# Kernel tuning notes

Hardware: AMD Instinct MI355X
Metric: run time of the kernel (lower is better)

The kernel has to match this reference:

```python
import jax, jax.numpy as jnp
import numpy as np

HEADS = 6
EPS = 1e-5


def _na_idx(L, k, d):
    # NATTEN-style dilated neighborhood: work within dilation cosets,
    # clamp window to stay inside the image (window shifts at borders).
    i = np.arange(L)
    g = i % d
    p = i // d
    Lg = (L - g + d - 1) // d  # coset length per position
    start = np.clip(p - k // 2, 0, Lg - k)
    j = np.arange(k)
    nbr = g[:, None] + d * (start[:, None] + j[None, :])          # [L,k] neighbor coords
    rel = (start[:, None] + j[None, :]) - p[:, None] + (k - 1)    # [L,k] rpb index in [0,2k-2]
    return jnp.asarray(nbr, jnp.int32), jnp.asarray(rel, jnp.int32)


def _na2d(x, qkv_w, qkv_b, proj_w, proj_b, rpb, heads, k, d):
    # x: [B,H,W,C] NHWC neighborhood attention with relative positional bias
    B, H, W, C = x.shape
    dh = C // heads
    scale = dh ** -0.5
    qkv = (x @ qkv_w + qkv_b).reshape(B, H, W, 3, heads, dh)
    qkv = jnp.transpose(qkv, (3, 0, 4, 1, 2, 5))  # [3,B,h,H,W,dh]
    q, kk, v = qkv[0] * scale, qkv[1], qkv[2]
    nh, rh = _na_idx(H, k, d)
    nw, rw = _na_idx(W, k, d)

    def gather(t):  # [B,h,H,W,dh] -> [B,h,H,W,k,k,dh]
        t = t[:, :, nh]              # [B,h,H,k,W,dh]
        t = t[:, :, :, :, nw]        # [B,h,H,k,W,k,dh]
        return jnp.transpose(t, (0, 1, 2, 4, 3, 5, 6))

    kn, vn = gather(kk), gather(v)
    attn = jnp.einsum('bhxyd,bhxyijd->bhxyij', q, kn)  # [B,h,H,W,k,k]
    bias = rpb[:, rh]                  # [h,H,k,2k-1]
    bias = bias[:, :, :, rw]           # [h,H,k,W,k]
    bias = jnp.transpose(bias, (0, 1, 3, 2, 4))  # [h,H,W,k,k]
    attn = attn + bias[None]
    attn = jax.nn.softmax(attn.reshape(B, heads, H, W, k * k), axis=-1)
    attn = attn.reshape(B, heads, H, W, k, k)
    out = jnp.einsum('bhxyij,bhxyijd->bhxyd', attn, vn)
    out = jnp.transpose(out, (0, 2, 3, 1, 4)).reshape(B, H, W, C)
    return out @ proj_w + proj_b


def _rln(x, w, b, m1_w, m1_b, m2_w, m2_b):
    # Revised LayerNorm: normalize over (C,H,W) per sample; meta1/meta2 are 1x1 convs on std/mean
    mean = jnp.mean(x, axis=(1, 2, 3), keepdims=True)
    std = jnp.sqrt(jnp.mean((x - mean) ** 2, axis=(1, 2, 3), keepdims=True) + EPS)
    out = (x - mean) / std * w + b
    rescale = m1_w[None, :, None, None] * std + m1_b[None, :, None, None]
    rebias = m2_w[None, :, None, None] * mean + m2_b[None, :, None, None]
    return out, rescale, rebias


def _c11(x, w, b):  # 1x1 conv on NCHW == per-pixel linear
    return jnp.einsum('bchw,oc->bohw', x, w) + b[None, :, None, None]


def _gelu(x):
    return jax.nn.gelu(x, approximate=False)


def reference(x, ln_w, ln_b, m1_w, m1_b, m2_w, m2_b, qkv1_w, qkv1_b, proj1_w, proj1_b, rpb1, qkv2_w, qkv2_b, proj2_w, proj2_b, rpb2, mlp_w1, mlp_b1, mlp_w2, mlp_b2, bn_g, bn_b, bn_m, bn_v, pa_w1, pa_b1, pa_w2, pa_b2, ca_w1, ca_b1, ca_w2, ca_b2, m2a_w1, m2a_b1, m2a_w2, m2a_b2):
    # ---- NA block 1 (kernel 7, dilation 1) ----
    sc = x
    y, rs, rb = _rln(x, ln_w, ln_b, m1_w, m1_b, m2_w, m2_b)
    a = _na2d(jnp.transpose(y, (0, 2, 3, 1)), qkv1_w, qkv1_b, proj1_w, proj1_b, rpb1, HEADS, 7, 1)
    x = sc + jnp.transpose(a, (0, 3, 1, 2)) * rs + rb
    # ---- NA block 2 (kernel 5, dilation 8) ----
    sc = x
    y, rs, rb = _rln(x, ln_w, ln_b, m1_w, m1_b, m2_w, m2_b)
    a = _na2d(jnp.transpose(y, (0, 2, 3, 1)), qkv2_w, qkv2_b, proj2_w, proj2_b, rpb2, HEADS, 5, 8)
    x = sc + jnp.transpose(a, (0, 3, 1, 2)) * rs + rb
    # ---- MLP (source reuses the pre-attn2 shortcut `sc`) ----
    y, rs, rb = _rln(x, ln_w, ln_b, m1_w, m1_b, m2_w, m2_b)
    m = _c11(jax.nn.relu(_c11(y, mlp_w1, mlp_b1)), mlp_w2, mlp_b2)
    x = sc + m * rs + rb
    # ---- BN + pixel attention + channel attention + mlp2 ----
    sc = x
    inv = jax.lax.rsqrt(bn_v + EPS)
    y = (x - bn_m[None, :, None, None]) * (inv * bn_g)[None, :, None, None] + bn_b[None, :, None, None]
    pa = jax.nn.sigmoid(_c11(_gelu(_c11(y, pa_w1, pa_b1)), pa_w2, pa_b2))  # [B,1,H,W]
    y = pa * y
    gap = jnp.mean(y, axis=(2, 3), keepdims=True)
    ca = jax.nn.sigmoid(_c11(_gelu(_c11(gap, ca_w1, ca_b1)), ca_w2, ca_b2))  # [B,C,1,1]
    y = ca * y
    y = _c11(_gelu(_c11(y, m2a_w1, m2a_b1)), m2a_w2, m2a_b2)
    return sc + y


def setup_inputs() -> dict:
    key = jax.random.key(0)
    B, C, H, W, HID = 4, 96, 64, 64, 384
    ks = iter(jax.random.split(key, 48))

    def rn(shape, s=0.02):
        return jax.random.normal(next(ks), shape, jnp.float32) * s

    d = {}
    d['x'] = jax.random.normal(next(ks), (B, C, H, W), jnp.float32)
    d['ln_w'] = jnp.ones((1, C, 1, 1), jnp.float32)
    d['ln_b'] = jnp.zeros((1, C, 1, 1), jnp.float32)
    d['m1_w'] = rn((C,)); d['m1_b'] = jnp.ones((C,), jnp.float32)
    d['m2_w'] = rn((C,)); d['m2_b'] = jnp.zeros((C,), jnp.float32)
    d['qkv1_w'] = rn((C, 3 * C)); d['qkv1_b'] = jnp.zeros((3 * C,), jnp.float32)
    d['proj1_w'] = rn((C, C)); d['proj1_b'] = jnp.zeros((C,), jnp.float32)
    d['rpb1'] = rn((HEADS, 13, 13))
    d['qkv2_w'] = rn((C, 3 * C)); d['qkv2_b'] = jnp.zeros((3 * C,), jnp.float32)
    d['proj2_w'] = rn((C, C)); d['proj2_b'] = jnp.zeros((C,), jnp.float32)
    d['rpb2'] = rn((HEADS, 9, 9))
    d['mlp_w1'] = rn((HID, C)); d['mlp_b1'] = jnp.zeros((HID,), jnp.float32)
    d['mlp_w2'] = rn((C, HID)); d['mlp_b2'] = jnp.zeros((C,), jnp.float32)
    d['bn_g'] = jnp.ones((C,), jnp.float32); d['bn_b'] = jnp.zeros((C,), jnp.float32)
    d['bn_m'] = jnp.zeros((C,), jnp.float32); d['bn_v'] = jnp.ones((C,), jnp.float32)
    d['pa_w1'] = rn((C // 8, C)); d['pa_b1'] = jnp.zeros((C // 8,), jnp.float32)
    d['pa_w2'] = rn((1, C // 8)); d['pa_b2'] = jnp.zeros((1,), jnp.float32)
    d['ca_w1'] = rn((C, C)); d['ca_b1'] = jnp.zeros((C,), jnp.float32)
    d['ca_w2'] = rn((C, C)); d['ca_b2'] = jnp.zeros((C,), jnp.float32)
    d['m2a_w1'] = rn((C, C)); d['m2a_b1'] = jnp.zeros((C,), jnp.float32)
    d['m2a_w2'] = rn((C, C)); d['m2a_b2'] = jnp.zeros((C,), jnp.float32)
    return d
```

## Files before the change

kernel.cpp:

```cpp
#include <hip/hip_runtime.h>
#include <math.h>

#define CC 96
#define NP 4096
#define NHEADS 6
#define NELEMF 393216.0f
#define EPSF 1e-5f

typedef __attribute__((ext_vector_type(8))) short bf16x8;
typedef __attribute__((ext_vector_type(4))) float f32x4;
#define MFMA16(a,b,c) __builtin_amdgcn_mfma_f32_16x16x32_bf16(a,b,c,0,0,0)

#define WS_STATS 0
#define WQKV1  64
#define WQKV2  (WQKV1+13824)
#define WPROJ1 (WQKV2+13824)
#define WPROJ2 (WPROJ1+4608)
#define WMLP1  (WPROJ2+4608)
#define WMLP2  (WMLP1+18432)
#define WM2A1  (WMLP2+18432)
#define WM2A2  (WM2A1+4608)
#define WPA1T  (WM2A2+4608)
#define WBNS   (WPA1T+1152)
#define WS_YPM 84352
#define WS_Q   870784
#define WS_K   (WS_Q+786432)
#define WS_V   (WS_K+786432)
#define WS_ATTPM (WS_V+786432)
#define WS_X1  (WS_ATTPM+786432)
#define WS_X2  (WS_X1+1572864)
#define WS_X3  (WS_X2+1572864)
#define WS_PA  (WS_X3+1572864)
#define WS_GAP (WS_PA+16384)
#define WS_CA  (WS_GAP+384)

__device__ __forceinline__ float gelu_f(float x){
  return 0.5f * x * (1.0f + erff(x * 0.7071067811865476f));
}
__device__ __forceinline__ float sigmoid_f(float x){
  return 1.0f / (1.0f + __expf(-x));
}
__device__ __forceinline__ unsigned short bfr(float f){
  unsigned int u = __float_as_uint(f);
  u += 0x7fffu + ((u >> 16) & 1u);
  return (unsigned short)(u >> 16);
}
__device__ __forceinline__ unsigned int bfpack(float a, float b){
  return (unsigned int)bfr(a) | ((unsigned int)bfr(b) << 16);
}
__device__ __forceinline__ float bflo(unsigned int u){ return __uint_as_float(u << 16); }
__device__ __forceinline__ float bfhi(unsigned int u){ return __uint_as_float(u & 0xffff0000u); }
__device__ __forceinline__ void get_ms(const float* st, int b, float& mean, float& inv, float& stdv){
  float s = st[b], s2 = st[4+b];
  mean = s * (1.0f/NELEMF);
  float var = fmaxf(s2 * (1.0f/NELEMF) - mean*mean, 0.0f);
  stdv = sqrtf(var + EPSF);
  inv = 1.0f / stdv;
}

__global__ void stats_kernel(const float* __restrict__ src, float* __restrict__ st){
  int b = blockIdx.x / CC, c = blockIdx.x % CC;
  const float* p = src + (b*CC + c)*NP;
  float s = 0.f, s2 = 0.f;
  for(int i = threadIdx.x; i < NP; i += 256){ float v = p[i]; s += v; s2 = fmaf(v, v, s2); }
  for(int off = 32; off > 0; off >>= 1){ s += __shfl_down(s, off); s2 += __shfl_down(s2, off); }
  __shared__ float ls[8];
  int wid = threadIdx.x >> 6;
  if((threadIdx.x & 63) == 0){ ls[wid] = s; ls[4+wid] = s2; }
  __syncthreads();
  if(threadIdx.x == 0){
    atomicAdd(&st[b],   ls[0]+ls[1]+ls[2]+ls[3]);
    atomicAdd(&st[4+b], ls[4]+ls[5]+ls[6]+ls[7]);
  }
}

__global__ void prep_weights(const float* __restrict__ q1, const float* __restrict__ q2,
                             const float* __restrict__ p1, const float* __restrict__ p2,
                             const float* __restrict__ w1, const float* __restrict__ w2,
                             const float* __restrict__ a1, const float* __restrict__ a2,
                             const float* __restrict__ pw1,
                             const float* __restrict__ bg, const float* __restrict__ bb,
                             const float* __restrict__ bm, const float* __restrict__ bv,
                             float* __restrict__ ws){
  int gid = blockIdx.x*256 + threadIdx.x;
  if(gid < 27648){ int n = gid/96, c = gid%96; ((unsigned short*)(ws+WQKV1))[gid] = bfr(q1[c*288+n]); }
  else if(gid < 55296){ int g = gid-27648; int n = g/96, c = g%96; ((unsigned short*)(ws+WQKV2))[g] = bfr(q2[c*288+n]); }
  else if(gid < 64512){ int g = gid-55296; int n = g/96, c = g%96; ((unsigned short*)(ws+WPROJ1))[g] = bfr(p1[c*96+n]); }
  else if(gid < 73728){ int g = gid-64512; int n = g/96, c = g%96; ((unsigned short*)(ws+WPROJ2))[g] = bfr(p2[c*96+n]); }
  else if(gid < 110592){ int g = gid-73728; ((unsigned short*)(ws+WMLP1))[g] = bfr(w1[g]); }
  else if(gid < 147456){ int g = gid-110592; ((unsigned short*)(ws+WMLP2))[g] = bfr(w2[g]); }
  else if(gid < 156672){ int g = gid-147456; ((unsigned short*)(ws+WM2A1))[g] = bfr(a1[g]); }
  else if(gid < 165888){ int g = gid-156672; ((unsigned short*)(ws+WM2A2))[g] = bfr(a2[g]); }
  else if(gid < 167040){ int g = gid-165888; int c = g/12, h = g%12; ws[WPA1T + g] = pw1[h*96+c]; }
  else if(gid < 167136){ int c = gid-167040;
    float sc = rsqrtf(bv[c] + EPSF) * bg[c];
    ws[WBNS + c] = sc;
    ws[WBNS + 96 + c] = bb[c] - bm[c]*sc;
  }
}

__global__ void __launch_bounds__(256) ln_tr_kernel(
    const float* __restrict__ src, const float* __restrict__ st,
    const float* __restrict__ lnw, const float* __restrict__ lnb,
    unsigned int* __restrict__ dst){
  int px0 = blockIdx.x*64; int b = px0 >> 12; int pxl0 = px0 & 4095;
  float mean, inv, stdv; get_ms(st, b, mean, inv, stdv);
  __shared__ float T[96*67];
  for(int idx = threadIdx.x; idx < 96*64; idx += 256){
    int c = idx >> 6, p = idx & 63;
    float s = inv*lnw[c]; float o = lnb[c] - mean*s;
    T[c*67 + p] = fmaf(src[(b*96 + c)*NP + pxl0 + p], s, o);
  }
  __syncthreads();
  for(int idx = threadIdx.x; idx < 64*48; idx += 256){
    int row = idx/48, cd = idx%48;
    dst[(px0 + row)*48 + cd] = bfpack(T[(2*cd)*67 + row], T[(2*cd+1)*67 + row]);
  }
}

__global__ void __launch_bounds__(256) y3_tr_kernel(
    const float* __restrict__ x3, const float* __restrict__ bns,
    const float* __restrict__ pa, const float* __restrict__ ca,
    unsigned int* __restrict__ dst){
  int px0 = blockIdx.x*64; int b = px0 >> 12; int pxl0 = px0 & 4095;
  __shared__ float T[96*67];
  for(int idx = threadIdx.x; idx < 96*64; idx += 256){
    int c = idx >> 6, p = idx & 63;
    float v = fmaf(x3[(b*96 + c)*NP + pxl0 + p], bns[c], bns[96 + c]);
    T[c*67 + p] = v * ca[b*96 + c] * pa[px0 + p];
  }
  __syncthreads();
  for(int idx = threadIdx.x; idx < 64*48; idx += 256){
    int row = idx/48, cd = idx%48;
    dst[(px0 + row)*48 + cd] = bfpack(T[(2*cd)*67 + row], T[(2*cd+1)*67 + row]);
  }
}

template<int K>
__device__ __forceinline__ void mfma_tile(const unsigned short* __restrict__ A,
                                          const unsigned short* __restrict__ W,
                                          int m_base, int n_base, f32x4 acc[2][3]){
  int lane = threadIdx.x & 63;
  int ml = lane & 15, q = lane >> 4;
  const bf16x8* a0 = (const bf16x8*)(A + (size_t)(m_base + ml)*K + q*8);
  const bf16x8* a1 = (const bf16x8*)(A + (size_t)(m_base + 16 + ml)*K + q*8);
  const bf16x8* b0 = (const bf16x8*)(W + (n_base + ml)*K + q*8);
  const bf16x8* b1 = (const bf16x8*)(W + (n_base + 16 + ml)*K + q*8);
  const bf16x8* b2 = (const bf16x8*)(W + (n_base + 32 + ml)*K + q*8);
  #pragma unroll
  for(int ks = 0; ks < K/32; ++ks){
    bf16x8 av0 = a0[ks*4], av1 = a1[ks*4];
    bf16x8 bv0 = b0[ks*4], bv1 = b1[ks*4], bv2 = b2[ks*4];
    acc[0][0] = MFMA16(av0, bv0, acc[0][0]);
    acc[0][1] = MFMA16(av0, bv1, acc[0][1]);
    acc[0][2] = MFMA16(av0, bv2, acc[0][2]);
    acc[1][0] = MFMA16(av1, bv0, acc[1][0]);
    acc[1][1] = MFMA16(av1, bv1, acc[1][1]);
    acc[1][2] = MFMA16(av1, bv2, acc[1][2]);
  }
}

__global__ void __launch_bounds__(256) gemm_qkv_kernel(
    const unsigned short* __restrict__ ypm, const unsigned short* __restrict__ wT,
    const float* __restrict__ qb,
    unsigned short* __restrict__ qo, unsigned short* __restrict__ ko, unsigned short* __restrict__ vo){
  int w = threadIdx.x >> 6, lane = threadIdx.x & 63;
  int ml = lane & 15, q = lane >> 4;
  int m_base = blockIdx.x*128 + w*32;
  int n0 = blockIdx.y*48;
  f32x4 acc[2][3];
  f32x4 z = {0.f,0.f,0.f,0.f};
  #pragma unroll
  for(int f=0; f<2; ++f) for(int g=0; g<3; ++g) acc[f][g] = z;
  mfma_tile<96>(ypm, wT, m_base, n0, acc);
  #pragma unroll
  for(int g = 0; g < 3; ++g){
    int nfb = n0 + g*16;
    int t = nfb/96, head = (nfb%96) >> 4;
    float scale = (t == 0) ? 0.25f : 1.0f;
    unsigned short* dst = (t == 0) ? qo : (t == 1) ? ko : vo;
    float bias = qb[nfb + ml];
    #pragma unroll
    for(int f = 0; f < 2; ++f){
      #pragma unroll
      for(int r = 0; r < 4; ++r){
        int m = m_base + f*16 + q*4 + r;
        int b = m >> 12, pxl = m & 4095;
        dst[(((size_t)(b*NHEADS + head))*NP + pxl)*16 + ml] = bfr((acc[f][g][r] + bias)*scale);
      }
    }
  }
}

__global__ void __launch_bounds__(256) gemm_proj_kernel(
    const unsigned short* __restrict__ attpm, const unsigned short* __restrict__ wT,
    const float* __restrict__ pb, const float* __restrict__ scx, const float* __restrict__ st,
    const float* __restrict__ m1w, const float* __restrict__ m1b,
    const float* __restrict__ m2w, const float* __restrict__ m2b,
    float* __restrict__ dst, float* __restrict__ st_out){
  int w = threadIdx.x >> 6, lane = threadIdx.x & 63;
  int ml = lane & 15, q = lane >> 4;
  int m_base = blockIdx.x*128 + w*32;
  int n0 = blockIdx.y*48;
  f32x4 acc[2][3];
  f32x4 z = {0.f,0.f,0.f,0.f};
  #pragma unroll
  for(int f=0; f<2; ++f) for(int g=0; g<3; ++g) acc[f][g] = z;
  mfma_tile<96>(attpm, wT, m_base, n0, acc);
  __shared__ float T[48*133];
  #pragma unroll
  for(int f = 0; f < 2; ++f)
    #pragma unroll
    for(int g = 0; g < 3; ++g)
      #pragma unroll
      for(int r = 0; r < 4; ++r)
        T[(g*16 + ml)*133 + w*32 + f*16 + q*4 + r] = acc[f][g][r];
  __syncthreads();
  int b = (blockIdx.x*128) >> 12, pxl0 = (blockIdx.x*128) & 4095;
  float mean, inv, stdv; get_ms(st, b, mean, inv, stdv);
  float s = 0.f, s2 = 0.f;
  for(int idx = threadIdx.x; idx < 48*128; idx += 256){
    int row = idx >> 7, px = idx & 127;
    int n = n0 + row;
    float rsf = fmaf(m1w[n], stdv, m1b[n]);
    float rbf = fmaf(m2w[n], mean, m2b[n]);
    int ad = (b*CC + n)*NP + pxl0 + px;
    float val = scx[ad] + (T[row*133 + px] + pb[n])*rsf + rbf;
    dst[ad] = val;
    s += val; s2 = fmaf(val, val, s2);
  }
  for(int off = 32; off > 0; off >>= 1){ s += __shfl_down(s, off); s2 += __shfl_down(s2, off); }
  __shared__ float ls[8];
  int wid = threadIdx.x >> 6;
  if((threadIdx.x & 63) == 0){ ls[wid] = s; ls[4+wid] = s2; }
  __syncthreads();
  if(threadIdx.x == 0){
    atomicAdd(&st_out[b],   ls[0]+ls[1]+ls[2]+ls[3]);
    atomicAdd(&st_out[4+b], ls[4]+ls[5]+ls[6]+ls[7]);
  }
}

__global__ void __launch_bounds__(256) gemm_mlp1_kernel(
    const unsigned short* __restrict__ ypm, const unsigned short* __restrict__ wT,
    const float* __restrict__ b1, unsigned short* __restrict__ hid){
  int w = threadIdx.x >> 6, lane = threadIdx.x & 63;
  int ml = lane & 15, q = lane >> 4;
  int m_base = blockIdx.x*128 + w*32;
  int n0 = blockIdx.y*48;
  f32x4 acc[2][3];
  f32x4 z = {0.f,0.f,0.f,0.f};
  #pragma unroll
  for(int f=0; f<2; ++f) for(int g=0; g<3; ++g) acc[f][g] = z;
  mfma_tile<96>(ypm, wT, m_base, n0, acc);
  #pragma unroll
  for(int g = 0; g < 3; ++g){
    int n = n0 + g*16 + ml;
    float bias = b1[n];
    #pragma unroll
    for(int f = 0; f < 2; ++f)
      #pragma unroll
      for(int r = 0; r < 4; ++r){
        int m = m_base + f*16 + q*4 + r;
        hid[(size_t)m*384 + n] = bfr(fmaxf(acc[f][g][r] + bias, 0.f));
      }
  }
}

__global__ void __launch_bounds__(256) gemm_mlp2_kernel(
    const unsigned short* __restrict__ hid, const unsigned short* __restrict__ wT,
    const float* __restrict__ b2, const float* __restrict__ scx, const float* __restrict__ st,
    const float* __restrict__ m1w, const float* __restrict__ m1b,
    const float* __restrict__ m2w, const float* __restrict__ m2b,
    float* __restrict__ dst){
  int w = threadIdx.x >> 6, lane = threadIdx.x & 63;
  int ml = lane & 15, q = lane >> 4;
  int m_base = blockIdx.x*128 + w*32;
  int n0 = blockIdx.y*48;
  f32x4 acc[2][3];
  f32x4 z = {0.f,0.f,0.f,0.f};
  #pragma unroll
  for(int f=0; f<2; ++f) for(int g=0; g<3; ++g) acc[f][g] = z;
  mfma_tile<384>(hid, wT, m_base, n0, acc);
  __shared__ float T[48*133];
  #pragma unroll
  for(int f = 0; f < 2; ++f)
    #pragma unroll
    for(int g = 0; g < 3; ++g)
      #pragma unroll
      for(int r = 0; r < 4; ++r)
        T[(g*16 + ml)*133 + w*32 + f*16 + q*4 + r] = acc[f][g][r];
  __syncthreads();
  int b = (blockIdx.x*128) >> 12, pxl0 = (blockIdx.x*128) & 4095;
  float mean, inv, stdv; get_ms(st, b, mean, inv, stdv);
  for(int idx = threadIdx.x; idx < 48*128; idx += 256){
    int row = idx >> 7, px = idx & 127;
    int n = n0 + row;
    float rsf = fmaf(m1w[n], stdv, m1b[n]);
    float rbf = fmaf(m2w[n], mean, m2b[n]);
    int ad = (b*CC + n)*NP + pxl0 + px;
    dst[ad] = scx[ad] + (T[row*133 + px] + b2[n])*rsf + rbf;
  }
}

__global__ void __launch_bounds__(256) gemm_m2a_kernel(
    const unsigned short* __restrict__ y3pm,
    const unsigned short* __restrict__ w1T, const float* __restrict__ b1,
    const unsigned short* __restrict__ w2T, const float* __restrict__ b2,
    const float* __restrict__ scx, float* __restrict__ outp){
  __shared__ __align__(16) char smbuf[128*104*2];
  unsigned short* tl = (unsigned short*)smbuf;
  float* T = (float*)smbuf;
  int w = threadIdx.x >> 6, lane = threadIdx.x & 63;
  int ml = lane & 15, q = lane >> 4;
  int m_base = blockIdx.x*128 + w*32;
  f32x4 z = {0.f,0.f,0.f,0.f};
  f32x4 acc[2][6];
  #pragma unroll
  for(int f=0; f<2; ++f) for(int g=0; g<6; ++g) acc[f][g] = z;
  {
    const bf16x8* a0 = (const bf16x8*)(y3pm + (size_t)(m_base + ml)*96 + q*8);
    const bf16x8* a1 = (const bf16x8*)(y3pm + (size_t)(m_base + 16 + ml)*96 + q*8);
    #pragma unroll
    for(int ks = 0; ks < 3; ++ks){
      bf16x8 av0 = a0[ks*4], av1 = a1[ks*4];
      #pragma unroll
      for(int g = 0; g < 6; ++g){
        bf16x8 bv = *(const bf16x8*)(w1T + (g*16 + ml)*96 + ks*32 + q*8);
        acc[0][g] = MFMA16(av0, bv, acc[0][g]);
        acc[1][g] = MFMA16(av1, bv, acc[1][g]);
      }
    }
  }
  #pragma unroll
  for(int g = 0; g < 6; ++g){
    float bias = b1[g*16 + ml];
    #pragma unroll
    for(int f = 0; f < 2; ++f)
      #pragma unroll
      for(int r = 0; r < 4; ++r)
        tl[(w*32 + f*16 + q*4 + r)*104 + g*16 + ml] = bfr(gelu_f(acc[f][g][r] + bias));
  }
  __syncthreads();
  f32x4 acc2[2][6];
  #pragma unroll
  for(int f=0; f<2; ++f) for(int g=0; g<6; ++g) acc2[f][g] = z;
  {
    const unsigned short* ar0 = tl + (w*32 + ml)*104;
    const unsigned short* ar1 = tl + (w*32 + 16 + ml)*104;
    #pragma unroll
    for(int ks = 0; ks < 3; ++ks){
      bf16x8 av0 = *(const bf16x8*)(ar0 + ks*32 + q*8);
      bf16x8 av1 = *(const bf16x8*)(ar1 + ks*32 + q*8);
      #pragma unroll
      for(int g = 0; g < 6; ++g){
        bf16x8 bv = *(const bf16x8*)(w2T + (g*16 + ml)*96 + ks*32 + q*8);
        acc2[0][g] = MFMA16(av0, bv, acc2[0][g]);
        acc2[1][g] = MFMA16(av1, bv, acc2[1][g]);
      }
    }
  }
  int b = (blockIdx.x*128) >> 12, pxl0 = (blockIdx.x*128) & 4095;
  #pragma unroll
  for(int half = 0; half < 2; ++half){
    __syncthreads();
    #pragma unroll
    for(int f = 0; f < 2; ++f)
      #pragma unroll
      for(int g = 0; g < 3; ++g)
        #pragma unroll
        for(int r = 0; r < 4; ++r)
          T[(g*16 + ml)*133 + w*32 + f*16 + q*4 + r] = acc2[f][half*3 + g][r];
    __syncthreads();
    for(int idx = threadIdx.x; idx < 48*128; idx += 256){
      int row = idx >> 7, px = idx & 127;
      int n = half*48 + row;
      int ad = (b*CC + n)*NP + pxl0 + px;
      outp[ad] = scx[ad] + T[row*133 + px] + b2[n];
    }
  }
}

template<int K, int D, int RPB>
__global__ void __launch_bounds__(256) attn_kernel(
    const unsigned short* __restrict__ qb, const unsigned short* __restrict__ kb,
    const unsigned short* __restrict__ vb, const float* __restrict__ rpb,
    unsigned short* __restrict__ outp){
  int bh = blockIdx.x >> 6;
  int x = blockIdx.x & 63;
  int head = bh % NHEADS, b = bh / NHEADS;

  int gx = x % D, px = x / D;
  int Lgx = (64 - gx + D - 1) / D;
  int sx = min(max(px - K/2, 0), Lgx - K);

  __shared__ unsigned int sm[2*K*512];
  unsigned int* kl = sm;
  unsigned int* vl = sm + K*512;
  const unsigned int* kg = (const unsigned int*)(kb + (size_t)bh*NP*16);
  const unsigned int* vg = (const unsigned int*)(vb + (size_t)bh*NP*16);
  int tid = threadIdx.x;
  #pragma unroll
  for(int i = 0; i < K; ++i){
    int hh = gx + D*(sx + i);
    ((uint2*)(kl + i*512))[tid] = ((const uint2*)(kg + hh*512))[tid];
    ((uint2*)(vl + i*512))[tid] = ((const uint2*)(vg + hh*512))[tid];
  }
  __syncthreads();

  int pixoff = tid >> 2, t = tid & 3;
  int y = pixoff;
  int pix = x*64 + y;
  uint2 qd = *(const uint2*)(qb + ((size_t)bh*NP + pix)*16 + 4*t);
  float qx = bflo(qd.x), qy = bfhi(qd.x), qz = bflo(qd.y), qw = bfhi(qd.y);

  int gy = y % D, py = y / D;
  int Lgy = (64 - gy + D - 1) / D;
  int sy = min(max(py - K/2, 0), Lgy - K);

  float sc[K*K];
  #pragma unroll
  for(int i = 0; i < K; ++i){
    #pragma unroll
    for(int j = 0; j < K; ++j){
      int ww = gy + D*(sy + j);
      uint2 kv = *(const uint2*)(kl + i*512 + ww*8 + t*2);
      float s = qx*bflo(kv.x);
      s = fmaf(qy, bfhi(kv.x), s);
      s = fmaf(qz, bflo(kv.y), s);
      s = fmaf(qw, bfhi(kv.y), s);
      sc[i*K + j] = s;
    }
  }
  float mx = -1e30f;
  #pragma unroll
  for(int i = 0; i < K; ++i){
    const float* brow = rpb + (head*RPB + (sx + i - px + (K-1)))*RPB + (sy - py + (K-1));
    #pragma unroll
    for(int j = 0; j < K; ++j){
      float s = sc[i*K + j];
      s += __shfl_xor(s, 1);
      s += __shfl_xor(s, 2);
      s += brow[j];
      sc[i*K + j] = s;
      mx = fmaxf(mx, s);
    }
  }
  float sum = 0.f;
  #pragma unroll
  for(int n = 0; n < K*K; ++n){ float e = __expf(sc[n] - mx); sc[n] = e; sum += e; }
  float rs = 1.0f / sum;
  float4 acc = {0,0,0,0};
  #pragma unroll
  for(int i = 0; i < K; ++i){
    #pragma unroll
    for(int j = 0; j < K; ++j){
      int ww = gy + D*(sy + j);
      float wgt = sc[i*K + j] * rs;
      uint2 vv = *(const uint2*)(vl + i*512 + ww*8 + t*2);
      acc.x = fmaf(wgt, bflo(vv.x), acc.x);
      acc.y = fmaf(wgt, bfhi(vv.x), acc.y);
      acc.z = fmaf(wgt, bflo(vv.y), acc.z);
      acc.w = fmaf(wgt, bfhi(vv.y), acc.w);
    }
  }
  ushort4 o4;
  o4.x = bfr(acc.x); o4.y = bfr(acc.y); o4.z = bfr(acc.z); o4.w = bfr(acc.w);
  *(ushort4*)(outp + ((size_t)(b*NP + pix))*96 + head*16 + 4*t) = o4;
}

__global__ void __launch_bounds__(256) pa_kernel(
    const float* __restrict__ x3, const float* __restrict__ bns,
    const float* __restrict__ w1t, const float* __restrict__ b1,
    const float* __restrict__ w2, const float* __restrict__ b2,
    float* __restrict__ pa){
  int b = blockIdx.x >> 4;
  int p = (blockIdx.x & 15)*256 + threadIdx.x;
  float acc[12];
  #pragma unroll
  for(int h = 0; h < 12; ++h) acc[h] = b1[h];
  #pragma unroll 8
  for(int c = 0; c < CC; ++c){
    float yv = fmaf(x3[(b*CC + c)*NP + p], bns[c], bns[96 + c]);
    #pragma unroll
    for(int h = 0; h < 12; ++h) acc[h] = fmaf(yv, w1t[c*12 + h], acc[h]);
  }
  float s = b2[0];
  #pragma unroll
  for(int h = 0; h < 12; ++h) s = fmaf(gelu_f(acc[h]), w2[h], s);
  pa[b*NP + p] = sigmoid_f(s);
}

__global__ void gap_kernel(const float* __restrict__ x3, const float* __restrict__ bns,
                           const float* __restrict__ pa, float* __restrict__ gap){
  int b = blockIdx.x / CC, c = blockIdx.x % CC;
  float scb = bns[c], shb = bns[96 + c];
  float s = 0.f;
  for(int i = threadIdx.x; i < NP; i += 256)
    s = fmaf(fmaf(x3[(b*CC + c)*NP + i], scb, shb), pa[b*NP + i], s);
  for(int off = 32; off > 0; off >>= 1) s += __shfl_down(s, off);
  __shared__ float ls[4];
  if((threadIdx.x & 63) == 0) ls[threadIdx.x >> 6] = s;
  __syncthreads();
  if(threadIdx.x == 0) gap[blockIdx.x] = (ls[0]+ls[1]+ls[2]+ls[3]) * (1.0f/4096.0f);
}

__global__ void ca_kernel(const float* __restrict__ gap, const float* __restrict__ w1,
                          const float* __restrict__ b1, const float* __restrict__ w2,
                          const float* __restrict__ b2, float* __restrict__ ca){
  int b = blockIdx.x; int o = threadIdx.x;
  __shared__ float g[96], t[96];
  if(o < 96) g[o] = gap[b*96 + o];
  __syncthreads();
  if(o < 96){
    float a = b1[o];
    for(int c = 0; c < 96; ++c) a = fmaf(g[c], w1[o*96 + c], a);
    t[o] = gelu_f(a);
  }
  __syncthreads();
  if(o < 96){
    float a = b2[o];
    for(int c = 0; c < 96; ++c) a = fmaf(t[c], w2[o*96 + c], a);
    ca[b*96 + o] = sigmoid_f(a);
  }
}

extern "C" void kernel_launch(void* const* d_in, const int* in_sizes, int n_in,
                              void* d_out, int out_size, void* d_ws, size_t ws_size,
                              hipStream_t stream){
  (void)in_sizes; (void)n_in; (void)out_size; (void)ws_size;
  const float* x     = (const float*)d_in[0];
  const float* lnw   = (const float*)d_in[1];
  const float* lnb   = (const float*)d_in[2];
  const float* m1w   = (const float*)d_in[3];
  const float* m1b   = (const float*)d_in[4];
  const float* m2w   = (const float*)d_in[5];
  const float* m2b   = (const float*)d_in[6];
  const float* qkv1w = (const float*)d_in[7];
  const float* qkv1b = (const float*)d_in[8];
  const float* proj1w= (const float*)d_in[9];
  const float* proj1b= (const float*)d_in[10];
  const float* rpb1  = (const float*)d_in[11];
  const float* qkv2w = (const float*)d_in[12];
  const float* qkv2b = (const float*)d_in[13];
  const float* proj2w= (const float*)d_in[14];
  const float* proj2b= (const float*)d_in[15];
  const float* rpb2  = (const float*)d_in[16];
  const float* mw1   = (const float*)d_in[17];
  const float* mb1   = (const float*)d_in[18];
  const float* mw2   = (const float*)d_in[19];
  const float* mb2   = (const float*)d_in[20];
  const float* bng   = (const float*)d_in[21];
  const float* bnb   = (const float*)d_in[22];
  const float* bnm   = (const float*)d_in[23];
  const float* bnv   = (const float*)d_in[24];
  const float* paw1  = (const float*)d_in[25];
  const float* pab1  = (const float*)d_in[26];
  const float* paw2  = (const float*)d_in[27];
  const float* pab2  = (const float*)d_in[28];
  const float* caw1  = (const float*)d_in[29];
  const float* cab1  = (const float*)d_in[30];
  const float* caw2  = (const float*)d_in[31];
  const float* cab2  = (const float*)d_in[32];
  const float* aw1   = (const float*)d_in[33];
  const float* ab1   = (const float*)d_in[34];
  const float* aw2   = (const float*)d_in[35];
  const float* ab2   = (const float*)d_in[36];

  float* ws  = (float*)d_ws;
  float* out = (float*)d_out;
  float* st0 = ws + WS_STATS;
  float* st1 = st0 + 8;
  float* st2 = st0 + 16;
  unsigned short* ypm   = (unsigned short*)(ws + WS_YPM);
  unsigned short* q     = (unsigned short*)(ws + WS_Q);
  unsigned short* k     = (unsigned short*)(ws + WS_K);
  unsigned short* v     = (unsigned short*)(ws + WS_V);
  unsigned short* attpm = (unsigned short*)(ws + WS_ATTPM);
  unsigned short* hid   = (unsigned short*)(ws + WS_Q);
  float* x1  = ws + WS_X1;
  float* x2  = ws + WS_X2;
  float* x3  = ws + WS_X3;
  float* pab = ws + WS_PA;
  float* gpb = ws + WS_GAP;
  float* cab = ws + WS_CA;
  float* bns = ws + WBNS;

  hipMemsetAsync(d_ws, 0, 64*sizeof(float), stream);
  prep_weights<<<653, 256, 0, stream>>>(qkv1w, qkv2w, proj1w, proj2w, mw1, mw2, aw1, aw2,
                                        paw1, bng, bnb, bnm, bnv, ws);

  stats_kernel<<<384, 256, 0, stream>>>(x, st0);
  ln_tr_kernel<<<256, 256, 0, stream>>>(x, st0, lnw, lnb, (unsigned int*)ypm);
  gemm_qkv_kernel<<<dim3(128,6), 256, 0, stream>>>(ypm, (unsigned short*)(ws+WQKV1), qkv1b, q, k, v);
  attn_kernel<7,1,13><<<1536, 256, 0, stream>>>(q, k, v, rpb1, attpm);
  gemm_proj_kernel<<<dim3(128,2), 256, 0, stream>>>(attpm, (unsigned short*)(ws+WPROJ1), proj1b,
                                                    x, st0, m1w, m1b, m2w, m2b, x1, st1);

  ln_tr_kernel<<<256, 256, 0, stream>>>(x1, st1, lnw, lnb, (unsigned int*)ypm);
  gemm_qkv_kernel<<<dim3(128,6), 256, 0, stream>>>(ypm, (unsigned short*)(ws+WQKV2), qkv2b, q, k, v);
  attn_kernel<5,8,9><<<1536, 256, 0, stream>>>(q, k, v, rpb2, attpm);
  gemm_proj_kernel<<<dim3(128,2), 256, 0, stream>>>(attpm, (unsigned short*)(ws+WPROJ2), proj2b,
                                                    x1, st1, m1w, m1b, m2w, m2b, x2, st2);

  ln_tr_kernel<<<256, 256, 0, stream>>>(x2, st2, lnw, lnb, (unsigned int*)ypm);
  gemm_mlp1_kernel<<<dim3(128,8), 256, 0, stream>>>(ypm, (unsigned short*)(ws+WMLP1), mb1, hid);
  gemm_mlp2_kernel<<<dim3(128,2), 256, 0, stream>>>(hid, (unsigned short*)(ws+WMLP2), mb2,
                                                    x1, st2, m1w, m1b, m2w, m2b, x3);

  pa_kernel<<<64, 256, 0, stream>>>(x3, bns, ws + WPA1T, pab1, paw2, pab2, pab);
  gap_kernel<<<384, 256, 0, stream>>>(x3, bns, pab, gpb);
  ca_kernel<<<4, 128, 0, stream>>>(gpb, caw1, cab1, caw2, cab2, cab);
  y3_tr_kernel<<<256, 256, 0, stream>>>(x3, bns, pab, cab, (unsigned int*)ypm);
  gemm_m2a_kernel<<<128, 256, 0, stream>>>(ypm, (unsigned short*)(ws+WM2A1), ab1,
                                           (unsigned short*)(ws+WM2A2), ab2, x3, out);
}
```

Before: 305.5 us.

## Fuse layernorm/transpose into GEMM prologues and merge PA with GAP

Removes the separate ln_tr and y3_tr transpose kernels. The QKV, MLP1 and M2A GEMMs now normalise the NCHW float input and stage it as bf16 in shared memory, with each block covering 64 pixels across all output columns. The PA and GAP kernels are merged, with GAP accumulated through wave shuffles and atomics into a buffer zeroed by a new memset. This cuts launches and intermediate global round trips, but each GEMM block now loops over every N tile with fewer blocks, and the GAP reduction becomes atomic, so summation order can vary.

```diff
diff --git a/kernel.cpp b/kernel.cpp
--- a/kernel.cpp
+++ b/kernel.cpp
@@ -22,7 +22,6 @@
 #define WM2A2  (WM2A1+4608)
 #define WPA1T  (WM2A2+4608)
 #define WBNS   (WPA1T+1152)
-#define WS_YPM 84352
 #define WS_Q   870784
 #define WS_K   (WS_Q+786432)
 #define WS_V   (WS_K+786432)
@@ -44,9 +43,6 @@
   unsigned int u = __float_as_uint(f);
   u += 0x7fffu + ((u >> 16) & 1u);
   return (unsigned short)(u >> 16);
-}
-__device__ __forceinline__ unsigned int bfpack(float a, float b){
-  return (unsigned int)bfr(a) | ((unsigned int)bfr(b) << 16);
 }
 __device__ __forceinline__ float bflo(unsigned int u){ return __uint_as_float(u << 16); }
 __device__ __forceinline__ float bfhi(unsigned int u){ return __uint_as_float(u & 0xffff0000u); }
@@ -99,94 +95,53 @@
   }
 }
 
-__global__ void __launch_bounds__(256) ln_tr_kernel(
-    const float* __restrict__ src, const float* __restrict__ st,
+__global__ void __launch_bounds__(256) gemm_qkv_kernel(
+    const float* __restrict__ xin, const float* __restrict__ st,
     const float* __restrict__ lnw, const float* __restrict__ lnb,
-    unsigned int* __restrict__ dst){
-  int px0 = blockIdx.x*64; int b = px0 >> 12; int pxl0 = px0 & 4095;
+    const unsigned short* __restrict__ wT, const float* __restrict__ qb,
+    unsigned short* __restrict__ qo, unsigned short* __restrict__ ko, unsigned short* __restrict__ vo){
+  __shared__ unsigned short Atl[64*104];
+  __shared__ float scl[96], ofs[96];
+  int m_base = blockIdx.x*64;
+  int b = m_base >> 12, pxl0 = m_base & 4095;
   float mean, inv, stdv; get_ms(st, b, mean, inv, stdv);
-  __shared__ float T[96*67];
-  for(int idx = threadIdx.x; idx < 96*64; idx += 256){
+  int tid = threadIdx.x;
+  if(tid < 96){ float s = inv*lnw[tid]; scl[tid] = s; ofs[tid] = lnb[tid] - mean*s; }
+  __syncthreads();
+  const float* src = xin + (size_t)b*CC*NP + pxl0;
+  for(int idx = tid; idx < 96*64; idx += 256){
     int c = idx >> 6, p = idx & 63;
-    float s = inv*lnw[c]; float o = lnb[c] - mean*s;
-    T[c*67 + p] = fmaf(src[(b*96 + c)*NP + pxl0 + p], s, o);
-  }
-  __syncthreads();
-  for(int idx = threadIdx.x; idx < 64*48; idx += 256){
-    int row = idx/48, cd = idx%48;
-    dst[(px0 + row)*48 + cd] = bfpack(T[(2*cd)*67 + row], T[(2*cd+1)*67 + row]);
-  }
-}
-
-__global__ void __launch_bounds__(256) y3_tr_kernel(
-    const float* __restrict__ x3, const float* __restrict__ bns,
-    const float* __restrict__ pa, const float* __restrict__ ca,
-    unsigned int* __restrict__ dst){
-  int px0 = blockIdx.x*64; int b = px0 >> 12; int pxl0 = px0 & 4095;
-  __shared__ float T[96*67];
-  for(int idx = threadIdx.x; idx < 96*64; idx += 256){
-    int c = idx >> 6, p = idx & 63;
-    float v = fmaf(x3[(b*96 + c)*NP + pxl0 + p], bns[c], bns[96 + c]);
-    T[c*67 + p] = v * ca[b*96 + c] * pa[px0 + p];
-  }
-  __syncthreads();
-  for(int idx = threadIdx.x; idx < 64*48; idx += 256){
-    int row = idx/48, cd = idx%48;
-    dst[(px0 + row)*48 + cd] = bfpack(T[(2*cd)*67 + row], T[(2*cd+1)*67 + row]);
-  }
-}
-
-template<int K>
-__device__ __forceinline__ void mfma_tile(const unsigned short* __restrict__ A,
-                                          const unsigned short* __restrict__ W,
-                                          int m_base, int n_base, f32x4 acc[2][3]){
-  int lane = threadIdx.x & 63;
-  int ml = lane & 15, q = lane >> 4;
-  const bf16x8* a0 = (const bf16x8*)(A + (size_t)(m_base + ml)*K + q*8);
-  const bf16x8* a1 = (const bf16x8*)(A + (size_t)(m_base + 16 + ml)*K + q*8);
-  const bf16x8* b0 = (const bf16x8*)(W + (n_base + ml)*K + q*8);
-  const bf16x8* b1 = (const bf16x8*)(W + (n_base + 16 + ml)*K + q*8);
-  const bf16x8* b2 = (const bf16x8*)(W + (n_base + 32 + ml)*K + q*8);
-  #pragma unroll
-  for(int ks = 0; ks < K/32; ++ks){
-    bf16x8 av0 = a0[ks*4], av1 = a1[ks*4];
-    bf16x8 bv0 = b0[ks*4], bv1 = b1[ks*4], bv2 = b2[ks*4];
-    acc[0][0] = MFMA16(av0, bv0, acc[0][0]);
-    acc[0][1] = MFMA16(av0, bv1, acc[0][1]);
-    acc[0][2] = MFMA16(av0, bv2, acc[0][2]);
-    acc[1][0] = MFMA16(av1, bv0, acc[1][0]);
-    acc[1][1] = MFMA16(av1, bv1, acc[1][1]);
-    acc[1][2] = MFMA16(av1, bv2, acc[1][2]);
-  }
-}
-
-__global__ void __launch_bounds__(256) gemm_qkv_kernel(
-    const unsigned short* __restrict__ ypm, const unsigned short* __restrict__ wT,
-    const float* __restrict__ qb,
-    unsigned short* __restrict__ qo, unsigned short* __restrict__ ko, unsigned short* __restrict__ vo){
-  int w = threadIdx.x >> 6, lane = threadIdx.x & 63;
-  int ml = lane & 15, q = lane >> 4;
-  int m_base = blockIdx.x*128 + w*32;
-  int n0 = blockIdx.y*48;
-  f32x4 acc[2][3];
+    Atl[p*104 + c] = bfr(fmaf(src[c*NP + p], scl[c], ofs[c]));
+  }
+  __syncthreads();
+  int w = tid >> 6, lane = tid & 63, ml = lane & 15, q = lane >> 4;
+  const unsigned short* arow = Atl + (w*16 + ml)*104;
+  bf16x8 av[3];
+  #pragma unroll
+  for(int ks = 0; ks < 3; ++ks) av[ks] = *(const bf16x8*)(arow + ks*32 + q*8);
   f32x4 z = {0.f,0.f,0.f,0.f};
   #pragma unroll
-  for(int f=0; f<2; ++f) for(int g=0; g<3; ++g) acc[f][g] = z;
-  mfma_tile<96>(ypm, wT, m_base, n0, acc);
-  #pragma unroll
-  for(int g = 0; g < 3; ++g){
-    int nfb = n0 + g*16;
-    int t = nfb/96, head = (nfb%96) >> 4;
-    float scale = (t == 0) ? 0.25f : 1.0f;
-    unsigned short* dst = (t == 0) ? qo : (t == 1) ? ko : vo;
-    float bias = qb[nfb + ml];
-    #pragma unroll
-    for(int f = 0; f < 2; ++f){
+  for(int g = 0; g < 6; ++g){
+    f32x4 acc[3] = {z, z, z};
+    #pragma unroll
+    for(int ks = 0; ks < 3; ++ks){
+      #pragma unroll
+      for(int gg = 0; gg < 3; ++gg){
+        bf16x8 bv = *(const bf16x8*)(wT + (g*48 + gg*16 + ml)*96 + ks*32 + q*8);
+        acc[gg] = MFMA16(av[ks], bv, acc[gg]);
+      }
+    }
+    #pragma unroll
+    for(int gg = 0; gg < 3; ++gg){
+      int nfb = g*48 + gg*16;
+      int t = nfb/96, head = (nfb%96) >> 4;
+      float scale = (t == 0) ? 0.25f : 1.0f;
+      unsigned short* dst = (t == 0) ? qo : (t == 1) ? ko : vo;
+      float bias = qb[nfb + ml];
       #pragma unroll
       for(int r = 0; r < 4; ++r){
-        int m = m_base + f*16 + q*4 + r;
-        int b = m >> 12, pxl = m & 4095;
-        dst[(((size_t)(b*NHEADS + head))*NP + pxl)*16 + ml] = bfr((acc[f][g][r] + bias)*scale);
+        int pxl = pxl0 + w*16 + q*4 + r;
+        dst[(((size_t)(b*NHEADS + head))*NP + pxl)*16 + ml] = bfr((acc[gg][r] + bias)*scale);
       }
     }
   }
@@ -206,7 +161,20 @@
   f32x4 z = {0.f,0.f,0.f,0.f};
   #pragma unroll
   for(int f=0; f<2; ++f) for(int g=0; g<3; ++g) acc[f][g] = z;
-  mfma_tile<96>(attpm, wT, m_base, n0, acc);
+  {
+    const bf16x8* a0 = (const bf16x8*)(attpm + (size_t)(m_base + ml)*96 + q*8);
+    const bf16x8* a1 = (const bf16x8*)(attpm + (size_t)(m_base + 16 + ml)*96 + q*8);
+    #pragma unroll
+    for(int ks = 0; ks < 3; ++ks){
+      bf16x8 av0 = a0[ks*4], av1 = a1[ks*4];
+      #pragma unroll
+      for(int g = 0; g < 3; ++g){
+        bf16x8 bv = *(const bf16x8*)(wT + (n0 + g*16 + ml)*96 + ks*32 + q*8);
+        acc[0][g] = MFMA16(av0, bv, acc[0][g]);
+        acc[1][g] = MFMA16(av1, bv, acc[1][g]);
+      }
+    }
+  }
   __shared__ float T[48*133];
   #pragma unroll
   for(int f = 0; f < 2; ++f)
@@ -241,28 +209,51 @@
 }
 
 __global__ void __launch_bounds__(256) gemm_mlp1_kernel(
-    const unsigned short* __restrict__ ypm, const unsigned short* __restrict__ wT,
-    const float* __restrict__ b1, unsigned short* __restrict__ hid){
-  int w = threadIdx.x >> 6, lane = threadIdx.x & 63;
-  int ml = lane & 15, q = lane >> 4;
-  int m_base = blockIdx.x*128 + w*32;
-  int n0 = blockIdx.y*48;
-  f32x4 acc[2][3];
+    const float* __restrict__ xin, const float* __restrict__ st,
+    const float* __restrict__ lnw, const float* __restrict__ lnb,
+    const unsigned short* __restrict__ wT, const float* __restrict__ b1,
+    unsigned short* __restrict__ hid){
+  __shared__ unsigned short Atl[64*104];
+  __shared__ float scl[96], ofs[96];
+  int m_base = blockIdx.x*64;
+  int b = m_base >> 12, pxl0 = m_base & 4095;
+  float mean, inv, stdv; get_ms(st, b, mean, inv, stdv);
+  int tid = threadIdx.x;
+  if(tid < 96){ float s = inv*lnw[tid]; scl[tid] = s; ofs[tid] = lnb[tid] - mean*s; }
+  __syncthreads();
+  const float* src = xin + (size_t)b*CC*NP + pxl0;
+  for(int idx = tid; idx < 96*64; idx += 256){
+    int c = idx >> 6, p = idx & 63;
+    Atl[p*104 + c] = bfr(fmaf(src[c*NP + p], scl[c], ofs[c]));
+  }
+  __syncthreads();
+  int w = tid >> 6, lane = tid & 63, ml = lane & 15, q = lane >> 4;
+  const unsigned short* arow = Atl + (w*16 + ml)*104;
+  bf16x8 av[3];
+  #pragma unroll
+  for(int ks = 0; ks < 3; ++ks) av[ks] = *(const bf16x8*)(arow + ks*32 + q*8);
   f32x4 z = {0.f,0.f,0.f,0.f};
   #pragma unroll
-  for(int f=0; f<2; ++f) for(int g=0; g<3; ++g) acc[f][g] = z;
-  mfma_tile<96>(ypm, wT, m_base, n0, acc);
-  #pragma unroll
-  for(int g = 0; g < 3; ++g){
-    int n = n0 + g*16 + ml;
-    float bias = b1[n];
-    #pragma unroll
-    for(int f = 0; f < 2; ++f)
+  for(int g = 0; g < 8; ++g){
+    f32x4 acc[3] = {z, z, z};
+    #pragma unroll
+    for(int ks = 0; ks < 3; ++ks){
+      #pragma unroll
+      for(int gg = 0; gg < 3; ++gg){
+        bf16x8 bv = *(const bf16x8*)(wT + (g*48 + gg*16 + ml)*96 + ks*32 + q*8);
+        acc[gg] = MFMA16(av[ks], bv, acc[gg]);
+      }
+    }
+    #pragma unroll
+    for(int gg = 0; gg < 3; ++gg){
+      int n = g*48 + gg*16 + ml;
+      float bias = b1[n];
       #pragma unroll
       for(int r = 0; r < 4; ++r){
-        int m = m_base + f*16 + q*4 + r;
-        hid[(size_t)m*384 + n] = bfr(fmaxf(acc[f][g][r] + bias, 0.f));
-      }
+        int m = m_base + w*16 + q*4 + r;
+        hid[(size_t)m*384 + n] = bfr(fmaxf(acc[gg][r] + bias, 0.f));
+      }
+    }
   }
 }
 
@@ -280,7 +271,20 @@
   f32x4 z = {0.f,0.f,0.f,0.f};
   #pragma unroll
   for(int f=0; f<2; ++f) for(int g=0; g<3; ++g) acc[f][g] = z;
-  mfma_tile<384>(hid, wT, m_base, n0, acc);
+  {
+    const bf16x8* a0 = (const bf16x8*)(hid + (size_t)(m_base + ml)*384 + q*8);
+    const bf16x8* a1 = (const bf16x8*)(hid + (size_t)(m_base + 16 + ml)*384 + q*8);
+    #pragma unroll
+    for(int ks = 0; ks < 12; ++ks){
+      bf16x8 av0 = a0[ks*4], av1 = a1[ks*4];
+      #pragma unroll
+      for(int g = 0; g < 3; ++g){
+        bf16x8 bv = *(const bf16x8*)(wT + (n0 + g*16 + ml)*384 + ks*32 + q*8);
+        acc[0][g] = MFMA16(av0, bv, acc[0][g]);
+        acc[1][g] = MFMA16(av1, bv, acc[1][g]);
+      }
+    }
+  }
   __shared__ float T[48*133];
   #pragma unroll
   for(int f = 0; f < 2; ++f)
@@ -303,31 +307,42 @@
 }
 
 __global__ void __launch_bounds__(256) gemm_m2a_kernel(
-    const unsigned short* __restrict__ y3pm,
+    const float* __restrict__ x3, const float* __restrict__ bns,
+    const float* __restrict__ pa, const float* __restrict__ ca,
     const unsigned short* __restrict__ w1T, const float* __restrict__ b1,
     const unsigned short* __restrict__ w2T, const float* __restrict__ b2,
     const float* __restrict__ scx, float* __restrict__ outp){
-  __shared__ __align__(16) char smbuf[128*104*2];
-  unsigned short* tl = (unsigned short*)smbuf;
+  __shared__ __align__(16) char smbuf[26624];
+  __shared__ float scl[96], ofs[96], pal[64];
+  unsigned short* Atl = (unsigned short*)smbuf;
+  unsigned short* tl2 = (unsigned short*)(smbuf + 13312);
   float* T = (float*)smbuf;
-  int w = threadIdx.x >> 6, lane = threadIdx.x & 63;
-  int ml = lane & 15, q = lane >> 4;
-  int m_base = blockIdx.x*128 + w*32;
+  int m_base = blockIdx.x*64;
+  int b = m_base >> 12, pxl0 = m_base & 4095;
+  int tid = threadIdx.x;
+  if(tid < 96){ float cv = ca[b*96 + tid]; scl[tid] = bns[tid]*cv; ofs[tid] = bns[96+tid]*cv; }
+  if(tid >= 128 && tid < 192) pal[tid-128] = pa[m_base + (tid-128)];
+  __syncthreads();
+  const float* src = x3 + (size_t)b*CC*NP + pxl0;
+  for(int idx = tid; idx < 96*64; idx += 256){
+    int c = idx >> 6, p = idx & 63;
+    Atl[p*104 + c] = bfr(fmaf(src[c*NP + p], scl[c], ofs[c]) * pal[p]);
+  }
+  __syncthreads();
+  int w = tid >> 6, lane = tid & 63, ml = lane & 15, q = lane >> 4;
   f32x4 z = {0.f,0.f,0.f,0.f};
-  f32x4 acc[2][6];
-  #pragma unroll
-  for(int f=0; f<2; ++f) for(int g=0; g<6; ++g) acc[f][g] = z;
+  f32x4 acc1[6];
+  #pragma unroll
+  for(int g=0; g<6; ++g) acc1[g] = z;
   {
-    const bf16x8* a0 = (const bf16x8*)(y3pm + (size_t)(m_base + ml)*96 + q*8);
-    const bf16x8* a1 = (const bf16x8*)(y3pm + (size_t)(m_base + 16 + ml)*96 + q*8);
+    const unsigned short* arow = Atl + (w*16 + ml)*104;
     #pragma unroll
     for(int ks = 0; ks < 3; ++ks){
-      bf16x8 av0 = a0[ks*4], av1 = a1[ks*4];
+      bf16x8 av = *(const bf16x8*)(arow + ks*32 + q*8);
       #pragma unroll
       for(int g = 0; g < 6; ++g){
         bf16x8 bv = *(const bf16x8*)(w1T + (g*16 + ml)*96 + ks*32 + q*8);
-        acc[0][g] = MFMA16(av0, bv, acc[0][g]);
-        acc[1][g] = MFMA16(av1, bv, acc[1][g]);
+        acc1[g] = MFMA16(av, bv, acc1[g]);
       }
     }
   }
@@ -335,48 +350,36 @@
   for(int g = 0; g < 6; ++g){
     float bias = b1[g*16 + ml];
     #pragma unroll
-    for(int f = 0; f < 2; ++f)
-      #pragma unroll
-      for(int r = 0; r < 4; ++r)
-        tl[(w*32 + f*16 + q*4 + r)*104 + g*16 + ml] = bfr(gelu_f(acc[f][g][r] + bias));
-  }
-  __syncthreads();
-  f32x4 acc2[2][6];
-  #pragma unroll
-  for(int f=0; f<2; ++f) for(int g=0; g<6; ++g) acc2[f][g] = z;
+    for(int r = 0; r < 4; ++r)
+      tl2[(w*16 + q*4 + r)*104 + g*16 + ml] = bfr(gelu_f(acc1[g][r] + bias));
+  }
+  __syncthreads();
+  f32x4 acc2[6];
+  #pragma unroll
+  for(int g=0; g<6; ++g) acc2[g] = z;
   {
-    const unsigned short* ar0 = tl + (w*32 + ml)*104;
-    const unsigned short* ar1 = tl + (w*32 + 16 + ml)*104;
+    const unsigned short* arow = tl2 + (w*16 + ml)*104;
     #pragma unroll
     for(int ks = 0; ks < 3; ++ks){
-      bf16x8 av0 = *(const bf16x8*)(ar0 + ks*32 + q*8);
-      bf16x8 av1 = *(const bf16x8*)(ar1 + ks*32 + q*8);
+      bf16x8 av = *(const bf16x8*)(arow + ks*32 + q*8);
       #pragma unroll
       for(int g = 0; g < 6; ++g){
         bf16x8 bv = *(const bf16x8*)(w2T + (g*16 + ml)*96 + ks*32 + q*8);
-        acc2[0][g] = MFMA16(av0, bv, acc2[0][g]);
-        acc2[1][g] = MFMA16(av1, bv, acc2[1][g]);
-      }
-    }
-  }
-  int b = (blockIdx.x*128) >> 12, pxl0 = (blockIdx.x*128) & 4095;
-  #pragma unroll
-  for(int half = 0; half < 2; ++half){
-    __syncthreads();
-    #pragma unroll
-    for(int f = 0; f < 2; ++f)
-      #pragma unroll
-      for(int g = 0; g < 3; ++g)
-        #pragma unroll
-        for(int r = 0; r < 4; ++r)
-          T[(g*16 + ml)*133 + w*32 + f*16 + q*4 + r] = acc2[f][half*3 + g][r];
-    __syncthreads();
-    for(int idx = threadIdx.x; idx < 48*128; idx += 256){
-      int row = idx >> 7, px = idx & 127;
-      int n = half*48 + row;
-      int ad = (b*CC + n)*NP + pxl0 + px;
-      outp[ad] = scx[ad] + T[row*133 + px] + b2[n];
-    }
+        acc2[g] = MFMA16(av, bv, acc2[g]);
+      }
+    }
+  }
+  __syncthreads();
+  #pragma unroll
+  for(int g = 0; g < 6; ++g)
+    #pragma unroll
+    for(int r = 0; r < 4; ++r)
+      T[(g*16 + ml)*68 + w*16 + q*4 + r] = acc2[g][r];
+  __syncthreads();
+  for(int idx = tid; idx < 96*64; idx += 256){
+    int n = idx >> 6, p = idx & 63;
+    int ad = (b*CC + n)*NP + pxl0 + p;
+    outp[ad] = scx[ad] + T[n*68 + p] + b2[n];
   }
 }
 
@@ -468,11 +471,11 @@
   *(ushort4*)(outp + ((size_t)(b*NP + pix))*96 + head*16 + 4*t) = o4;
 }
 
-__global__ void __launch_bounds__(256) pa_kernel(
+__global__ void __launch_bounds__(256) pa_gap_kernel(
     const float* __restrict__ x3, const float* __restrict__ bns,
     const float* __restrict__ w1t, const float* __restrict__ b1,
     const float* __restrict__ w2, const float* __restrict__ b2,
-    float* __restrict__ pa){
+    float* __restrict__ pa, float* __restrict__ gap){
   int b = blockIdx.x >> 4;
   int p = (blockIdx.x & 15)*256 + threadIdx.x;
   float acc[12];
@@ -487,21 +490,20 @@
   float s = b2[0];
   #pragma unroll
   for(int h = 0; h < 12; ++h) s = fmaf(gelu_f(acc[h]), w2[h], s);
-  pa[b*NP + p] = sigmoid_f(s);
-}
-
-__global__ void gap_kernel(const float* __restrict__ x3, const float* __restrict__ bns,
-                           const float* __restrict__ pa, float* __restrict__ gap){
-  int b = blockIdx.x / CC, c = blockIdx.x % CC;
-  float scb = bns[c], shb = bns[96 + c];
-  float s = 0.f;
-  for(int i = threadIdx.x; i < NP; i += 256)
-    s = fmaf(fmaf(x3[(b*CC + c)*NP + i], scb, shb), pa[b*NP + i], s);
-  for(int off = 32; off > 0; off >>= 1) s += __shfl_down(s, off);
-  __shared__ float ls[4];
-  if((threadIdx.x & 63) == 0) ls[threadIdx.x >> 6] = s;
-  __syncthreads();
-  if(threadIdx.x == 0) gap[blockIdx.x] = (ls[0]+ls[1]+ls[2]+ls[3]) * (1.0f/4096.0f);
+  float pav = sigmoid_f(s);
+  pa[b*NP + p] = pav;
+  __shared__ float gpart[4*96];
+  int lane = threadIdx.x & 63, wid = threadIdx.x >> 6;
+  for(int c = 0; c < CC; ++c){
+    float t = fmaf(x3[(b*CC + c)*NP + p], bns[c], bns[96 + c]) * pav;
+    t += __shfl_xor(t, 1);  t += __shfl_xor(t, 2);  t += __shfl_xor(t, 4);
+    t += __shfl_xor(t, 8);  t += __shfl_xor(t, 16); t += __shfl_xor(t, 32);
+    if(lane == 0) gpart[wid*96 + c] = t;
+  }
+  __syncthreads();
+  for(int c = threadIdx.x; c < CC; c += 256)
+    atomicAdd(&gap[b*96 + c],
+              (gpart[c] + gpart[96+c] + gpart[192+c] + gpart[288+c]) * (1.0f/4096.0f));
 }
 
 __global__ void ca_kernel(const float* __restrict__ gap, const float* __restrict__ w1,
@@ -571,7 +573,6 @@
   float* st0 = ws + WS_STATS;
   float* st1 = st0 + 8;
   float* st2 = st0 + 16;
-  unsigned short* ypm   = (unsigned short*)(ws + WS_YPM);
   unsigned short* q     = (unsigned short*)(ws + WS_Q);
   unsigned short* k     = (unsigned short*)(ws + WS_K);
   unsigned short* v     = (unsigned short*)(ws + WS_V);
@@ -586,31 +587,27 @@
   float* bns = ws + WBNS;
 
   hipMemsetAsync(d_ws, 0, 64*sizeof(float), stream);
+  hipMemsetAsync((void*)(ws + WS_GAP), 0, 384*sizeof(float), stream);
   prep_weights<<<653, 256, 0, stream>>>(qkv1w, qkv2w, proj1w, proj2w, mw1, mw2, aw1, aw2,
                                         paw1, bng, bnb, bnm, bnv, ws);
 
   stats_kernel<<<384, 256, 0, stream>>>(x, st0);
-  ln_tr_kernel<<<256, 256, 0, stream>>>(x, st0, lnw, lnb, (unsigned int*)ypm);
-  gemm_qkv_kernel<<<dim3(128,6), 256, 0, stream>>>(ypm, (unsigned short*)(ws+WQKV1), qkv1b, q, k, v);
+  gemm_qkv_kernel<<<256, 256, 0, stream>>>(x, st0, lnw, lnb, (unsigned short*)(ws+WQKV1), qkv1b, q, k, v);
   attn_kernel<7,1,13><<<1536, 256, 0, stream>>>(q, k, v, rpb1, attpm);
   gemm_proj_kernel<<<dim3(128,2), 256, 0, stream>>>(attpm, (unsigned short*)(ws+WPROJ1), proj1b,
                                                     x, st0, m1w, m1b, m2w, m2b, x1, st1);
 
-  ln_tr_kernel<<<256, 256, 0, stream>>>(x1, st1, lnw, lnb, (unsigned int*)ypm);
-  gemm_qkv_kernel<<<dim3(128,6), 256, 0, stream>>>(ypm, (unsigned short*)(ws+WQKV2), qkv2b, q, k, v);
+  gemm_qkv_kernel<<<256, 256, 0, stream>>>(x1, st1, lnw, lnb, (unsigned short*)(ws+WQKV2), qkv2b, q, k, v);
   attn_kernel<5,8,9><<<1536, 256, 0, stream>>>(q, k, v, rpb2, attpm);
   gemm_proj_kernel<<<dim3(128,2), 256, 0, stream>>>(attpm, (unsigned short*)(ws+WPROJ2), proj2b,
                                                     x1, st1, m1w, m1b, m2w, m2b, x2, st2);
 
-  ln_tr_kernel<<<256, 256, 0, stream>>>(x2, st2, lnw, lnb, (unsigned int*)ypm);
-  gemm_mlp1_kernel<<<dim3(128,8), 256, 0, stream>>>(ypm, (unsigned short*)(ws+WMLP1), mb1, hid);
+  gemm_mlp1_kernel<<<256, 256, 0, stream>>>(x2, st2, lnw, lnb, (unsigned short*)(ws+WMLP1), mb1, hid);
   gemm_mlp2_kernel<<<dim3(128,2), 256, 0, stream>>>(hid, (unsigned short*)(ws+WMLP2), mb2,
                                                     x1, st2, m1w, m1b, m2w, m2b, x3);
 
-  pa_kernel<<<64, 256, 0, stream>>>(x3, bns, ws + WPA1T, pab1, paw2, pab2, pab);
-  gap_kernel<<<384, 256, 0, stream>>>(x3, bns, pab, gpb);
+  pa_gap_kernel<<<64, 256, 0, stream>>>(x3, bns, ws + WPA1T, pab1, paw2, pab2, pab, gpb);
   ca_kernel<<<4, 128, 0, stream>>>(gpb, caw1, cab1, caw2, cab2, cab);
-  y3_tr_kernel<<<256, 256, 0, stream>>>(x3, bns, pab, cab, (unsigned int*)ypm);
-  gemm_m2a_kernel<<<128, 256, 0, stream>>>(ypm, (unsigned short*)(ws+WM2A1), ab1,
+  gemm_m2a_kernel<<<256, 256, 0, stream>>>(x3, bns, pab, cab, (unsigned short*)(ws+WM2A1), ab1,
                                            (unsigned short*)(ws+WM2A2), ab2, x3, out);
 }
```

After: 323.3 us. +5.8%, slower.
